# Optimization experiments

Measured on AMD Instinct MI355X. Metric: run time of the kernel, lower is better.

The kernel has to match this reference:

```python
import jax, jax.numpy as jnp
import numpy as np

I = 512  # input_size
H = 512  # hidden_size
L = 512  # sequence length
N = 64   # batch


def setup_inputs() -> dict:
    key = jax.random.key(0)
    ks = jax.random.split(key, 12)
    s_ih = 1.0 / np.sqrt(H)
    inp = {
        "input": jax.random.normal(ks[0], (L, N, I), dtype=jnp.float32),
        "h_0": jax.random.normal(ks[1], (2, N, H), dtype=jnp.float32),
        # layer 0 params
        "W_ih_l0": jax.random.uniform(ks[2], (H, I), jnp.float32, -s_ih, s_ih),
        "W_hh_l0": jax.random.uniform(ks[3], (H, H), jnp.float32, -s_ih, s_ih),
        "b_ih_l0": jax.random.uniform(ks[4], (H,), jnp.float32, -s_ih, s_ih),
        "b_hh_l0": jax.random.uniform(ks[5], (H,), jnp.float32, -s_ih, s_ih),
        # layer 1 params (input is layer 0 hidden state, size H)
        "W_ih_l1": jax.random.uniform(ks[6], (H, H), jnp.float32, -s_ih, s_ih),
        "W_hh_l1": jax.random.uniform(ks[7], (H, H), jnp.float32, -s_ih, s_ih),
        "b_ih_l1": jax.random.uniform(ks[8], (H,), jnp.float32, -s_ih, s_ih),
        "b_hh_l1": jax.random.uniform(ks[9], (H,), jnp.float32, -s_ih, s_ih),
    }
    return inp


def reference(input, h_0, W_ih_l0, W_hh_l0, b_ih_l0, b_hh_l0,
              W_ih_l1, W_hh_l1, b_ih_l1, b_hh_l1):
    """2-layer Elman RNN with tanh: h[t] = tanh(x[t] W_ih^T + b_ih + h[t-1] W_hh^T + b_hh).
    Layer 1 consumes layer 0's hidden state at the same timestep.
    Returns (output: (L, N, H), h_n: (2, N, H)).
    """

    def step(carry, x_t):
        h0, h1 = carry  # each (N, H)
        h0_new = jnp.tanh(x_t @ W_ih_l0.T + b_ih_l0 + h0 @ W_hh_l0.T + b_hh_l0)
        h1_new = jnp.tanh(h0_new @ W_ih_l1.T + b_ih_l1 + h1 @ W_hh_l1.T + b_hh_l1)
        return (h0_new, h1_new), h1_new

    (h0_n, h1_n), output = jax.lax.scan(step, (h_0[0], h_0[1]), input)
    h_n = jnp.stack([h0_n, h1_n], axis=0)
    return output, h_n
```

## Files before the change

kernel.cpp:

```cpp
#include <hip/hip_runtime.h>
#include <hip/hip_bf16.h>
#include <math.h>

#define L_SEQ 512
#define N_B   64
#define H_D   512
#define M_TOT (L_SEQ * N_B)

typedef unsigned short u16;
typedef unsigned long long u64;
typedef __attribute__((ext_vector_type(8))) short short8;
typedef __attribute__((ext_vector_type(4))) float f32x4;
typedef __attribute__((ext_vector_type(4))) int i32x4;
typedef __attribute__((ext_vector_type(2))) int i32x2;

__device__ __forceinline__ u16 f2bf(float f) {
    unsigned int u = __builtin_bit_cast(unsigned int, f);
    u = u + 0x7fffu + ((u >> 16) & 1u);
    return (u16)(u >> 16);
}

__device__ __forceinline__ float fast_tanh(float x) {
    float e = __expf(2.0f * x);
    return 1.0f - 2.0f / (e + 1.0f);
}

__device__ __forceinline__ void st_h(u16* p, u16 v) {
    __hip_atomic_store(p, v, __ATOMIC_RELAXED, __HIP_MEMORY_SCOPE_AGENT);
}
__device__ __forceinline__ void st_flag(int* p, int v) {
    __hip_atomic_store(p, v, __ATOMIC_RELAXED, __HIP_MEMORY_SCOPE_AGENT);
}

#define FSTRIDE 16

#define LD16(f, p)                                                          \
  asm volatile(                                                             \
    "global_load_dwordx4 %0, %16, off\n\t"                                  \
    "global_load_dwordx4 %1, %16, off offset:64\n\t"                        \
    "global_load_dwordx4 %2, %16, off offset:128\n\t"                       \
    "global_load_dwordx4 %3, %16, off offset:192\n\t"                       \
    "global_load_dwordx4 %4, %16, off offset:256\n\t"                       \
    "global_load_dwordx4 %5, %16, off offset:320\n\t"                       \
    "global_load_dwordx4 %6, %16, off offset:384\n\t"                       \
    "global_load_dwordx4 %7, %16, off offset:448\n\t"                       \
    "global_load_dwordx4 %8, %16, off offset:512\n\t"                       \
    "global_load_dwordx4 %9, %16, off offset:576\n\t"                       \
    "global_load_dwordx4 %10, %16, off offset:640\n\t"                      \
    "global_load_dwordx4 %11, %16, off offset:704\n\t"                      \
    "global_load_dwordx4 %12, %16, off offset:768\n\t"                      \
    "global_load_dwordx4 %13, %16, off offset:832\n\t"                      \
    "global_load_dwordx4 %14, %16, off offset:896\n\t"                      \
    "global_load_dwordx4 %15, %16, off offset:960\n\t"                      \
    "s_waitcnt vmcnt(0)"                                                    \
    : "=&v"(f[0]), "=&v"(f[1]), "=&v"(f[2]), "=&v"(f[3]),                   \
      "=&v"(f[4]), "=&v"(f[5]), "=&v"(f[6]), "=&v"(f[7]),                   \
      "=&v"(f[8]), "=&v"(f[9]), "=&v"(f[10]), "=&v"(f[11]),                 \
      "=&v"(f[12]), "=&v"(f[13]), "=&v"(f[14]), "=&v"(f[15])                \
    : "v"(p) : "memory")

#define LD16X2(f, g, p0, p1)                                                \
  asm volatile(                                                             \
    "global_load_dwordx4 %0, %32, off\n\t"                                  \
    "global_load_dwordx4 %16, %33, off\n\t"                                 \
    "global_load_dwordx4 %1, %32, off offset:64\n\t"                        \
    "global_load_dwordx4 %17, %33, off offset:64\n\t"                       \
    "global_load_dwordx4 %2, %32, off offset:128\n\t"                       \
    "global_load_dwordx4 %18, %33, off offset:128\n\t"                      \
    "global_load_dwordx4 %3, %32, off offset:192\n\t"                       \
    "global_load_dwordx4 %19, %33, off offset:192\n\t"                      \
    "global_load_dwordx4 %4, %32, off offset:256\n\t"                       \
    "global_load_dwordx4 %20, %33, off offset:256\n\t"                      \
    "global_load_dwordx4 %5, %32, off offset:320\n\t"                       \
    "global_load_dwordx4 %21, %33, off offset:320\n\t"                      \
    "global_load_dwordx4 %6, %32, off offset:384\n\t"                       \
    "global_load_dwordx4 %22, %33, off offset:384\n\t"                      \
    "global_load_dwordx4 %7, %32, off offset:448\n\t"                       \
    "global_load_dwordx4 %23, %33, off offset:448\n\t"                      \
    "global_load_dwordx4 %8, %32, off offset:512\n\t"                       \
    "global_load_dwordx4 %24, %33, off offset:512\n\t"                      \
    "global_load_dwordx4 %9, %32, off offset:576\n\t"                       \
    "global_load_dwordx4 %25, %33, off offset:576\n\t"                      \
    "global_load_dwordx4 %10, %32, off offset:640\n\t"                      \
    "global_load_dwordx4 %26, %33, off offset:640\n\t"                      \
    "global_load_dwordx4 %11, %32, off offset:704\n\t"                      \
    "global_load_dwordx4 %27, %33, off offset:704\n\t"                      \
    "global_load_dwordx4 %12, %32, off offset:768\n\t"                      \
    "global_load_dwordx4 %28, %33, off offset:768\n\t"                      \
    "global_load_dwordx4 %13, %32, off offset:832\n\t"                      \
    "global_load_dwordx4 %29, %33, off offset:832\n\t"                      \
    "global_load_dwordx4 %14, %32, off offset:896\n\t"                      \
    "global_load_dwordx4 %30, %33, off offset:896\n\t"                      \
    "global_load_dwordx4 %15, %32, off offset:960\n\t"                      \
    "global_load_dwordx4 %31, %33, off offset:960\n\t"                      \
    "s_waitcnt vmcnt(0)"                                                    \
    : "=&v"(f[0]), "=&v"(f[1]), "=&v"(f[2]), "=&v"(f[3]),                   \
      "=&v"(f[4]), "=&v"(f[5]), "=&v"(f[6]), "=&v"(f[7]),                   \
      "=&v"(f[8]), "=&v"(f[9]), "=&v"(f[10]), "=&v"(f[11]),                 \
      "=&v"(f[12]), "=&v"(f[13]), "=&v"(f[14]), "=&v"(f[15]),               \
      "=&v"(g[0]), "=&v"(g[1]), "=&v"(g[2]), "=&v"(g[3]),                   \
      "=&v"(g[4]), "=&v"(g[5]), "=&v"(g[6]), "=&v"(g[7]),                   \
      "=&v"(g[8]), "=&v"(g[9]), "=&v"(g[10]), "=&v"(g[11]),                 \
      "=&v"(g[12]), "=&v"(g[13]), "=&v"(g[14]), "=&v"(g[15])                \
    : "v"(p0), "v"(p1) : "memory")

#define WAITVM asm volatile("s_waitcnt vmcnt(0)" ::: "memory")

__device__ __host__ __forceinline__ int perm32(int j) {
    return (((j >> 3) & 3) << 2) | (j & 3) | (((j >> 2) & 1) << 4);
}

__global__ void k_prep(const float* __restrict__ x,
                       const float* __restrict__ w0ih, const float* __restrict__ w0hh,
                       const float* __restrict__ b0i,  const float* __restrict__ b0h,
                       const float* __restrict__ w1ih, const float* __restrict__ w1hh,
                       const float* __restrict__ b1i,  const float* __restrict__ b1h,
                       u16* __restrict__ xb,
                       u16* __restrict__ w0ihb, u16* __restrict__ w0hhb,
                       u16* __restrict__ w1ihb, u16* __restrict__ w1hhb,
                       float* __restrict__ bias0, float* __restrict__ bias1,
                       int* __restrict__ flags)
{
    const int stride = gridDim.x * blockDim.x;
    const int tid = blockIdx.x * blockDim.x + threadIdx.x;
    for (int i = tid; i < M_TOT * H_D / 4; i += stride) {
        const float4 v = ((const float4*)x)[i];
        ushort4 o;
        o.x = f2bf(v.x); o.y = f2bf(v.y); o.z = f2bf(v.z); o.w = f2bf(v.w);
        ((ushort4*)xb)[i] = o;
    }
    for (int i = tid; i < H_D * H_D; i += stride) {
        const int p  = i & (H_D - 1);
        const int pc = (i & ~(H_D - 1)) | (p & ~31) | perm32(p & 31);
        w0ihb[i] = f2bf(w0ih[i]);
        w0hhb[i] = f2bf(w0hh[pc]);
        w1ihb[i] = f2bf(w1ih[pc]);
        w1hhb[i] = f2bf(w1hh[i]);
    }
    if (tid < H_D) {
        bias0[tid] = b0i[tid] + b0h[tid];
        bias1[tid] = b1i[tid] + b1h[tid];
    }
    if (tid < 48 * FSTRIDE) flags[tid] = 0;
}

__global__ __launch_bounds__(256)
void k_gemm(const u16* __restrict__ A, const u16* __restrict__ W,
            const float* __restrict__ bias, float* __restrict__ out)
{
    __shared__ u16 As[128][40];
    __shared__ u16 Ws[128][40];
    const int m0 = blockIdx.x * 128;
    const int n0 = blockIdx.y * 128;
    const int tid = threadIdx.x;
    const int w = tid >> 6, l = tid & 63, q = l >> 4, lr = l & 15;
    const int mw = (w >> 1) * 64, nw = (w & 1) * 64;
    const int skg = (tid & 3) * 8;
    const int smr = tid >> 2;

    f32x4 acc[4][4];
    #pragma unroll
    for (int i = 0; i < 4; ++i)
        #pragma unroll
        for (int j = 0; j < 4; ++j)
            acc[i][j] = (f32x4){0.f, 0.f, 0.f, 0.f};

    for (int kk = 0; kk < H_D; kk += 32) {
        *(uint4*)&As[smr][skg]      = *(const uint4*)(A + (size_t)(m0 + smr) * H_D + kk + skg);
        *(uint4*)&As[smr + 64][skg] = *(const uint4*)(A + (size_t)(m0 + smr + 64) * H_D + kk + skg);
        *(uint4*)&Ws[smr][skg]      = *(const uint4*)(W + (size_t)(n0 + smr) * H_D + kk + skg);
        *(uint4*)&Ws[smr + 64][skg] = *(const uint4*)(W + (size_t)(n0 + smr + 64) * H_D + kk + skg);
        __syncthreads();
        short8 af[4], bf[4];
        #pragma unroll
        for (int rt = 0; rt < 4; ++rt) af[rt] = *(const short8*)&As[mw + rt*16 + lr][q*8];
        #pragma unroll
        for (int nt = 0; nt < 4; ++nt) bf[nt] = *(const short8*)&Ws[nw + nt*16 + lr][q*8];
        #pragma unroll
        for (int rt = 0; rt < 4; ++rt)
            #pragma unroll
            for (int nt = 0; nt < 4; ++nt)
                acc[rt][nt] = __builtin_amdgcn_mfma_f32_16x16x32_bf16(af[rt], bf[nt], acc[rt][nt], 0, 0, 0);
        __syncthreads();
    }
    #pragma unroll
    for (int nt = 0; nt < 4; ++nt) {
        const int col = n0 + nw + nt*16 + lr;
        const float bv = bias[col];
        #pragma unroll
        for (int rt = 0; rt < 4; ++rt) {
            #pragma unroll
            for (int r = 0; r < 4; ++r) {
                const int row = m0 + mw + rt*16 + q*4 + r;
                out[(size_t)row * H_D + col] = acc[rt][nt][r] + bv;
            }
        }
    }
}

__global__ __launch_bounds__(256, 1)
void k_rec_fused(const u16* __restrict__ Whh0, const u16* __restrict__ Wih1,
                 const u16* __restrict__ Whh1,
                 const float* __restrict__ h_init,
                 const float* __restrict__ pre0,
                 const float* __restrict__ bias1,
                 u16* __restrict__ h0buf, u16* __restrict__ h1buf,
                 float* __restrict__ out, float* __restrict__ hn,
                 int* __restrict__ flags0, int* __restrict__ flags1)
{
    (void)__hip_atomic_load(flags0, __ATOMIC_ACQUIRE, __HIP_MEMORY_SCOPE_AGENT);

    const int tid = threadIdx.x;
    const int w = tid >> 6, l = tid & 63, q = l >> 4, lr = l & 15;
    const int r0 = w * 16;
    const int m = r0 + lr;

    if (blockIdx.x < 16) {
        const int c = blockIdx.x;
        const int nbase = c * 32;
        short8 breg[16][2];
        #pragma unroll
        for (int kt = 0; kt < 16; ++kt)
            #pragma unroll
            for (int nt = 0; nt < 2; ++nt)
                breg[kt][nt] = *(const short8*)(Whh0 + (size_t)(nbase + nt*16 + lr) * H_D + kt*32 + q*8);

        #pragma unroll
        for (int j = 0; j < 8; ++j) {
            int idx = l * 8 + j;
            int row = r0 + (idx >> 5);
            int pos = idx & 31;
            st_h(h0buf + (size_t)row * H_D + nbase + pos,
                 f2bf(h_init[row * H_D + nbase + perm32(pos)]));
        }
        WAITVM;
        __syncthreads();
        if (tid == 0) st_flag(flags0 + c * FSTRIDE, 1);

        for (int t = 0; t < L_SEQ; ++t) {
            const float* pt = pre0 + (size_t)t * (N_B * H_D)
                            + (size_t)(r0 + lr) * H_D + nbase + q*4;
            f32x4 acc0a = *(const f32x4*)pt;
            f32x4 acc1a = *(const f32x4*)(pt + 16);
            f32x4 acc0b = (f32x4){0.f,0.f,0.f,0.f};
            f32x4 acc1b = (f32x4){0.f,0.f,0.f,0.f};
            f32x4 acc0c = (f32x4){0.f,0.f,0.f,0.f};
            f32x4 acc1c = (f32x4){0.f,0.f,0.f,0.f};
            f32x4 acc0d = (f32x4){0.f,0.f,0.f,0.f};
            f32x4 acc1d = (f32x4){0.f,0.f,0.f,0.f};

            if (w == 0) {
                const int* p = flags0 + (l & 15) * FSTRIDE;
                while (true) {
                    int v = __hip_atomic_load(p, __ATOMIC_RELAXED, __HIP_MEMORY_SCOPE_AGENT);
                    if (__all(v >= t + 1)) break;
                }
                asm volatile("" ::: "memory");
            }
            __syncthreads();

            const u16* hs = h0buf + ((size_t)t * N_B + m) * H_D + q*8;
            i32x4 f[16];
            LD16(f, hs);
            #pragma unroll
            for (int kt = 0; kt < 16; kt += 4) {
                acc0a = __builtin_amdgcn_mfma_f32_16x16x32_bf16(breg[kt][0],   __builtin_bit_cast(short8, f[kt]),   acc0a, 0, 0, 0);
                acc1a = __builtin_amdgcn_mfma_f32_16x16x32_bf16(breg[kt][1],   __builtin_bit_cast(short8, f[kt]),   acc1a, 0, 0, 0);
                acc0b = __builtin_amdgcn_mfma_f32_16x16x32_bf16(breg[kt+1][0], __builtin_bit_cast(short8, f[kt+1]), acc0b, 0, 0, 0);
                acc1b = __builtin_amdgcn_mfma_f32_16x16x32_bf16(breg[kt+1][1], __builtin_bit_cast(short8, f[kt+1]), acc1b, 0, 0, 0);
                acc0c = __builtin_amdgcn_mfma_f32_16x16x32_bf16(breg[kt+2][0], __builtin_bit_cast(short8, f[kt+2]), acc0c, 0, 0, 0);
                acc1c = __builtin_amdgcn_mfma_f32_16x16x32_bf16(breg[kt+2][1], __builtin_bit_cast(short8, f[kt+2]), acc1c, 0, 0, 0);
                acc0d = __builtin_amdgcn_mfma_f32_16x16x32_bf16(breg[kt+3][0], __builtin_bit_cast(short8, f[kt+3]), acc0d, 0, 0, 0);
                acc1d = __builtin_amdgcn_mfma_f32_16x16x32_bf16(breg[kt+3][1], __builtin_bit_cast(short8, f[kt+3]), acc1d, 0, 0, 0);
            }
            float v0[4], v1[4];
            #pragma unroll
            for (int r = 0; r < 4; ++r) {
                v0[r] = fast_tanh((acc0a[r] + acc0b[r]) + (acc0c[r] + acc0d[r]));
                v1[r] = fast_tanh((acc1a[r] + acc1b[r]) + (acc1c[r] + acc1d[r]));
            }
            i32x4 dd;
            dd[0] = (int)((unsigned)f2bf(v0[0]) | ((unsigned)f2bf(v0[1]) << 16));
            dd[1] = (int)((unsigned)f2bf(v0[2]) | ((unsigned)f2bf(v0[3]) << 16));
            dd[2] = (int)((unsigned)f2bf(v1[0]) | ((unsigned)f2bf(v1[1]) << 16));
            dd[3] = (int)((unsigned)f2bf(v1[2]) | ((unsigned)f2bf(v1[3]) << 16));
            u16* hd = h0buf + (size_t)(t+1) * (N_B * H_D)
                    + (size_t)(r0 + lr) * H_D + nbase + q*8;
            asm volatile(
                "global_store_dwordx4 %1, %0, off sc1"
                :: "v"(dd), "v"(hd) : "memory");
            WAITVM;
            __syncthreads();
            if (tid == 0) st_flag(flags0 + c * FSTRIDE, t + 2);

            if (t == L_SEQ - 1) {
                f32x4 o0 = {v0[0], v0[1], v0[2], v0[3]};
                f32x4 o1 = {v1[0], v1[1], v1[2], v1[3]};
                *(f32x4*)(hn + (size_t)(r0 + lr) * H_D + nbase + q*4)      = o0;
                *(f32x4*)(hn + (size_t)(r0 + lr) * H_D + nbase + 16 + q*4) = o1;
            }
        }
    } else {
        const int c = blockIdx.x - 16;
        const int nbase = c * 16;
        short8 bregI[16], bregH[16];
        #pragma unroll
        for (int kt = 0; kt < 16; ++kt) {
            bregI[kt] = *(const short8*)(Wih1 + (size_t)(nbase + lr) * H_D + kt*32 + q*8);
            bregH[kt] = *(const short8*)(Whh1 + (size_t)(nbase + lr) * H_D + kt*32 + q*8);
        }
        const f32x4 bv4 = *(const f32x4*)(bias1 + nbase + q*4);

        const float* hi1 = h_init + N_B * H_D;
        #pragma unroll
        for (int j = 0; j < 4; ++j) {
            int idx = l * 4 + j;
            int row = r0 + (idx >> 4);
            int col = nbase + (idx & 15);
            st_h(h1buf + (size_t)row * H_D + col, f2bf(hi1[row * H_D + col]));
        }
        WAITVM;
        __syncthreads();
        if (tid == 0) st_flag(flags1 + c * FSTRIDE, 1);

        for (int t = 0; t < L_SEQ; ++t) {
            if (w == 0) {
                const int* p;
                int need;
                if (l < 16)      { p = flags0 + l * FSTRIDE;        need = t + 2; }
                else if (l < 48) { p = flags1 + (l - 16) * FSTRIDE; need = t + 1; }
                else             { p = flags0;                      need = 0;     }
                while (true) {
                    int v = __hip_atomic_load(p, __ATOMIC_RELAXED, __HIP_MEMORY_SCOPE_AGENT);
                    if (__all(v >= need)) break;
                }
                asm volatile("" ::: "memory");
            }
            __syncthreads();

            const u16* p0 = h0buf + ((size_t)(t+1) * N_B + m) * H_D + q*8;
            const u16* p1 = h1buf + ((size_t)t     * N_B + m) * H_D + q*8;
            i32x4 f[16], g[16];
            LD16X2(f, g, p0, p1);
            f32x4 accA = bv4;
            f32x4 accB = (f32x4){0.f,0.f,0.f,0.f};
            f32x4 accC = (f32x4){0.f,0.f,0.f,0.f};
            f32x4 accD = (f32x4){0.f,0.f,0.f,0.f};
            #pragma unroll
            for (int kt = 0; kt < 16; kt += 2) {
                accA = __builtin_amdgcn_mfma_f32_16x16x32_bf16(bregI[kt],   __builtin_bit_cast(short8, f[kt]),   accA, 0, 0, 0);
                accB = __builtin_amdgcn_mfma_f32_16x16x32_bf16(bregH[kt],   __builtin_bit_cast(short8, g[kt]),   accB, 0, 0, 0);
                accC = __builtin_amdgcn_mfma_f32_16x16x32_bf16(bregI[kt+1], __builtin_bit_cast(short8, f[kt+1]), accC, 0, 0, 0);
                accD = __builtin_amdgcn_mfma_f32_16x16x32_bf16(bregH[kt+1], __builtin_bit_cast(short8, g[kt+1]), accD, 0, 0, 0);
            }
            float v[4];
            #pragma unroll
            for (int r = 0; r < 4; ++r)
                v[r] = fast_tanh((accA[r] + accB[r]) + (accC[r] + accD[r]));
            i32x2 d;
            d[0] = (int)((unsigned)f2bf(v[0]) | ((unsigned)f2bf(v[1]) << 16));
            d[1] = (int)((unsigned)f2bf(v[2]) | ((unsigned)f2bf(v[3]) << 16));
            u16* hd = h1buf + (size_t)(t+1) * (N_B * H_D)
                    + (size_t)(r0 + lr) * H_D + nbase + q*4;
            asm volatile(
                "global_store_dwordx2 %1, %0, off sc1"
                :: "v"(d), "v"(hd) : "memory");
            WAITVM;
            __syncthreads();
            if (tid == 0) st_flag(flags1 + c * FSTRIDE, t + 2);

            f32x4 ov = {v[0], v[1], v[2], v[3]};
            *(f32x4*)(out + (size_t)t * (N_B * H_D)
                      + (size_t)(r0 + lr) * H_D + nbase + q*4) = ov;
            if (t == L_SEQ - 1)
                *(f32x4*)(hn + (size_t)(N_B + r0 + lr) * H_D + nbase + q*4) = ov;
        }
    }
}

extern "C" void kernel_launch(void* const* d_in, const int* in_sizes, int n_in,
                              void* d_out, int out_size, void* d_ws, size_t ws_size,
                              hipStream_t stream)
{
    (void)in_sizes; (void)n_in; (void)out_size; (void)ws_size;
    const float* x    = (const float*)d_in[0];
    const float* h0   = (const float*)d_in[1];
    const float* w0ih = (const float*)d_in[2];
    const float* w0hh = (const float*)d_in[3];
    const float* b0i  = (const float*)d_in[4];
    const float* b0h  = (const float*)d_in[5];
    const float* w1ih = (const float*)d_in[6];
    const float* w1hh = (const float*)d_in[7];
    const float* b1i  = (const float*)d_in[8];
    const float* b1h  = (const float*)d_in[9];
    float* out = (float*)d_out;
    float* hn  = out + (size_t)M_TOT * H_D;

    char* ws = (char*)d_ws;
    size_t off = 0;
    u16* w0ihb = (u16*)(ws + off);   off += (size_t)H_D * H_D * 2;
    u16* w0hhb = (u16*)(ws + off);   off += (size_t)H_D * H_D * 2;
    u16* w1ihb = (u16*)(ws + off);   off += (size_t)H_D * H_D * 2;
    u16* w1hhb = (u16*)(ws + off);   off += (size_t)H_D * H_D * 2;
    float* bias0 = (float*)(ws + off); off += H_D * 4;
    float* bias1 = (float*)(ws + off); off += H_D * 4;
    int* flags   = (int*)(ws + off);   off += 48 * FSTRIDE * 4;
    int* flags0  = flags;
    int* flags1  = flags + 16 * FSTRIDE;
    u16* h0buf   = (u16*)(ws + off);   off += (size_t)(L_SEQ + 1) * N_B * H_D * 2;
    float* pre0  = (float*)(ws + off); off += (size_t)M_TOT * H_D * 4;
    u16* h1buf   = (u16*)(ws + off);   off += (size_t)(L_SEQ + 1) * N_B * H_D * 2;
    u16* xb      = h1buf;

    k_prep<<<2048, 256, 0, stream>>>(x, w0ih, w0hh, b0i, b0h, w1ih, w1hh, b1i, b1h,
                                     xb, w0ihb, w0hhb, w1ihb, w1hhb,
                                     bias0, bias1, flags);
    k_gemm<<<dim3(M_TOT/128, H_D/128), 256, 0, stream>>>(xb, w0ihb, bias0, pre0);
    k_rec_fused<<<48, 256, 0, stream>>>(w0hhb, w1ihb, w1hhb, h0, pre0, bias1,
                                        h0buf, h1buf, out, hn, flags0, flags1);
}
```

Before: 2.935 ms.

## Split recurrence by batch rows so each block owns full hidden state in LDS

Restructures the recurrent kernel so each 512-thread block handles 16 batch rows across all 512 hidden units. It keeps the hidden state in swizzled shared memory and W_hh in registers plus LDS, which removes the per-step cross-block flag waits inside each layer's recurrence. Layer 1's input projection moves to separate blocks that compute h0·W_ih1 into the pre0 buffer and signal through per-warp flags, pipelining the two layers. This trades a wide cross-block dependency every step for a longer serial per-block chain, fewer blocks (24), and heavy register and LDS use.

```diff
diff --git a/kernel.cpp b/kernel.cpp
--- a/kernel.cpp
+++ b/kernel.cpp
@@ -6,6 +6,8 @@
 #define N_B   64
 #define H_D   512
 #define M_TOT (L_SEQ * N_B)
+#define FSTRIDE 16
+#define SMEM_BYTES (16384 + 8 * 16384)
 
 typedef unsigned short u16;
 typedef unsigned long long u64;
@@ -31,8 +33,6 @@
 __device__ __forceinline__ void st_flag(int* p, int v) {
     __hip_atomic_store(p, v, __ATOMIC_RELAXED, __HIP_MEMORY_SCOPE_AGENT);
 }
-
-#define FSTRIDE 16
 
 #define LD16(f, p)                                                          \
   asm volatile(                                                             \
@@ -59,51 +59,6 @@
       "=&v"(f[12]), "=&v"(f[13]), "=&v"(f[14]), "=&v"(f[15])                \
     : "v"(p) : "memory")
 
-#define LD16X2(f, g, p0, p1)                                                \
-  asm volatile(                                                             \
-    "global_load_dwordx4 %0, %32, off\n\t"                                  \
-    "global_load_dwordx4 %16, %33, off\n\t"                                 \
-    "global_load_dwordx4 %1, %32, off offset:64\n\t"                        \
-    "global_load_dwordx4 %17, %33, off offset:64\n\t"                       \
-    "global_load_dwordx4 %2, %32, off offset:128\n\t"                       \
-    "global_load_dwordx4 %18, %33, off offset:128\n\t"                      \
-    "global_load_dwordx4 %3, %32, off offset:192\n\t"                       \
-    "global_load_dwordx4 %19, %33, off offset:192\n\t"                      \
-    "global_load_dwordx4 %4, %32, off offset:256\n\t"                       \
-    "global_load_dwordx4 %20, %33, off offset:256\n\t"                      \
-    "global_load_dwordx4 %5, %32, off offset:320\n\t"                       \
-    "global_load_dwordx4 %21, %33, off offset:320\n\t"                      \
-    "global_load_dwordx4 %6, %32, off offset:384\n\t"                       \
-    "global_load_dwordx4 %22, %33, off offset:384\n\t"                      \
-    "global_load_dwordx4 %7, %32, off offset:448\n\t"                       \
-    "global_load_dwordx4 %23, %33, off offset:448\n\t"                      \
-    "global_load_dwordx4 %8, %32, off offset:512\n\t"                       \
-    "global_load_dwordx4 %24, %33, off offset:512\n\t"                      \
-    "global_load_dwordx4 %9, %32, off offset:576\n\t"                       \
-    "global_load_dwordx4 %25, %33, off offset:576\n\t"                      \
-    "global_load_dwordx4 %10, %32, off offset:640\n\t"                      \
-    "global_load_dwordx4 %26, %33, off offset:640\n\t"                      \
-    "global_load_dwordx4 %11, %32, off offset:704\n\t"                      \
-    "global_load_dwordx4 %27, %33, off offset:704\n\t"                      \
-    "global_load_dwordx4 %12, %32, off offset:768\n\t"                      \
-    "global_load_dwordx4 %28, %33, off offset:768\n\t"                      \
-    "global_load_dwordx4 %13, %32, off offset:832\n\t"                      \
-    "global_load_dwordx4 %29, %33, off offset:832\n\t"                      \
-    "global_load_dwordx4 %14, %32, off offset:896\n\t"                      \
-    "global_load_dwordx4 %30, %33, off offset:896\n\t"                      \
-    "global_load_dwordx4 %15, %32, off offset:960\n\t"                      \
-    "global_load_dwordx4 %31, %33, off offset:960\n\t"                      \
-    "s_waitcnt vmcnt(0)"                                                    \
-    : "=&v"(f[0]), "=&v"(f[1]), "=&v"(f[2]), "=&v"(f[3]),                   \
-      "=&v"(f[4]), "=&v"(f[5]), "=&v"(f[6]), "=&v"(f[7]),                   \
-      "=&v"(f[8]), "=&v"(f[9]), "=&v"(f[10]), "=&v"(f[11]),                 \
-      "=&v"(f[12]), "=&v"(f[13]), "=&v"(f[14]), "=&v"(f[15]),               \
-      "=&v"(g[0]), "=&v"(g[1]), "=&v"(g[2]), "=&v"(g[3]),                   \
-      "=&v"(g[4]), "=&v"(g[5]), "=&v"(g[6]), "=&v"(g[7]),                   \
-      "=&v"(g[8]), "=&v"(g[9]), "=&v"(g[10]), "=&v"(g[11]),                 \
-      "=&v"(g[12]), "=&v"(g[13]), "=&v"(g[14]), "=&v"(g[15])                \
-    : "v"(p0), "v"(p1) : "memory")
-
 #define WAITVM asm volatile("s_waitcnt vmcnt(0)" ::: "memory")
 
 __device__ __host__ __forceinline__ int perm32(int j) {
@@ -133,7 +88,7 @@
         const int p  = i & (H_D - 1);
         const int pc = (i & ~(H_D - 1)) | (p & ~31) | perm32(p & 31);
         w0ihb[i] = f2bf(w0ih[i]);
-        w0hhb[i] = f2bf(w0hh[pc]);
+        w0hhb[i] = f2bf(w0hh[i]);
         w1ihb[i] = f2bf(w1ih[pc]);
         w1hhb[i] = f2bf(w1hh[i]);
     }
@@ -141,7 +96,7 @@
         bias0[tid] = b0i[tid] + b0h[tid];
         bias1[tid] = b1i[tid] + b1h[tid];
     }
-    if (tid < 48 * FSTRIDE) flags[tid] = 0;
+    if (tid < 192 * FSTRIDE) flags[tid] = 0;
 }
 
 __global__ __launch_bounds__(256)
@@ -198,182 +153,244 @@
     }
 }
 
-__global__ __launch_bounds__(256, 1)
-void k_rec_fused(const u16* __restrict__ Whh0, const u16* __restrict__ Wih1,
-                 const u16* __restrict__ Whh1,
-                 const float* __restrict__ h_init,
-                 const float* __restrict__ pre0,
-                 const float* __restrict__ bias1,
-                 u16* __restrict__ h0buf, u16* __restrict__ h1buf,
-                 float* __restrict__ out, float* __restrict__ hn,
-                 int* __restrict__ flags0, int* __restrict__ flags1)
+__global__ __launch_bounds__(512, 2)
+void k_rec(const u16* __restrict__ Whh0, const u16* __restrict__ Wih1p,
+           const u16* __restrict__ Whh1,
+           const float* __restrict__ h_init,
+           float* __restrict__ pre0,
+           const float* __restrict__ bias1,
+           u16* __restrict__ h0buf,
+           float* __restrict__ out, float* __restrict__ hn,
+           int* __restrict__ flags)
 {
-    (void)__hip_atomic_load(flags0, __ATOMIC_ACQUIRE, __HIP_MEMORY_SCOPE_AGENT);
+    extern __shared__ char smem[];
+    int* flag0 = flags;
+    int* flagF = flags + 16 * FSTRIDE;
+    (void)__hip_atomic_load(flags, __ATOMIC_ACQUIRE, __HIP_MEMORY_SCOPE_AGENT);
 
     const int tid = threadIdx.x;
     const int w = tid >> 6, l = tid & 63, q = l >> 4, lr = l & 15;
-    const int r0 = w * 16;
-    const int m = r0 + lr;
-
-    if (blockIdx.x < 16) {
-        const int c = blockIdx.x;
+    const int swz = (lr & 7) << 4;
+    const int blk = blockIdx.x;
+
+    if (blk < 4) {
+        const int b = blk;
+        const int R = b * 16;
+        short8 bregR[16][3];
+        #pragma unroll
+        for (int kt = 0; kt < 16; ++kt)
+            #pragma unroll
+            for (int nt = 0; nt < 3; ++nt)
+                bregR[kt][nt] = *(const short8*)(Whh0 + (size_t)(64*w + nt*16 + lr) * H_D + kt*32 + q*8);
+        char* wl = smem + 16384 + w * 16384;
+        #pragma unroll
+        for (int kt = 0; kt < 16; ++kt) {
+            short8 t3 = *(const short8*)(Whh0 + (size_t)(64*w + 48 + lr) * H_D + kt*32 + q*8);
+            *(short8*)(wl + kt*1024 + (size_t)l*16) = t3;
+        }
+        #pragma unroll
+        for (int j = 0; j < 16; ++j) {
+            int col = 64*w + q*16 + j;
+            *(u16*)(smem + (((size_t)lr*1024 + col*2) ^ swz)) =
+                f2bf(h_init[(R + lr) * H_D + col]);
+        }
+        __syncthreads();
+
+        f32x4 pr[4];
+        #pragma unroll
+        for (int nt = 0; nt < 4; ++nt)
+            pr[nt] = *(const f32x4*)(pre0 + (size_t)(R+lr)*H_D + 64*w + nt*16 + q*4);
+        f32x4 acc[4];
+        #pragma unroll
+        for (int nt = 0; nt < 4; ++nt) acc[nt] = (f32x4){0.f,0.f,0.f,0.f};
+
+        for (int t = 0; t < L_SEQ; ++t) {
+            #pragma unroll
+            for (int kt = 0; kt < 16; ++kt) {
+                short8 hf = *(const short8*)(smem + (((size_t)lr*1024 + kt*64 + q*16) ^ swz));
+                short8 wf = *(const short8*)(wl + kt*1024 + (size_t)l*16);
+                acc[0] = __builtin_amdgcn_mfma_f32_16x16x32_bf16(bregR[kt][0], hf, acc[0], 0,0,0);
+                acc[1] = __builtin_amdgcn_mfma_f32_16x16x32_bf16(bregR[kt][1], hf, acc[1], 0,0,0);
+                acc[2] = __builtin_amdgcn_mfma_f32_16x16x32_bf16(bregR[kt][2], hf, acc[2], 0,0,0);
+                acc[3] = __builtin_amdgcn_mfma_f32_16x16x32_bf16(wf,           hf, acc[3], 0,0,0);
+            }
+            __syncthreads();
+            if (tid == 0 && t > 0) st_flag(flag0 + b*FSTRIDE, t + 1);
+
+            float v[16]; unsigned hb[16];
+            #pragma unroll
+            for (int nt = 0; nt < 4; ++nt)
+                #pragma unroll
+                for (int r = 0; r < 4; ++r) {
+                    v[nt*4+r]  = fast_tanh(acc[nt][r] + pr[nt][r]);
+                    hb[nt*4+r] = f2bf(v[nt*4+r]);
+                }
+            #pragma unroll
+            for (int nt = 0; nt < 4; ++nt) {
+                i32x2 d;
+                d[0] = (int)(hb[nt*4]   | (hb[nt*4+1] << 16));
+                d[1] = (int)(hb[nt*4+2] | (hb[nt*4+3] << 16));
+                *(i32x2*)(smem + (((size_t)lr*1024 + (64*w + nt*16 + q*4)*2) ^ swz)) = d;
+            }
+            __syncthreads();
+
+            i32x4 dA, dB;
+            dA[0] = (int)(hb[0]  | (hb[1]  << 16)); dA[1] = (int)(hb[2]  | (hb[3]  << 16));
+            dA[2] = (int)(hb[4]  | (hb[5]  << 16)); dA[3] = (int)(hb[6]  | (hb[7]  << 16));
+            dB[0] = (int)(hb[8]  | (hb[9]  << 16)); dB[1] = (int)(hb[10] | (hb[11] << 16));
+            dB[2] = (int)(hb[12] | (hb[13] << 16)); dB[3] = (int)(hb[14] | (hb[15] << 16));
+            u16* hd = h0buf + (size_t)(t+1)*(N_B*H_D) + (size_t)(R+lr)*H_D + 64*w + q*8;
+            asm volatile("global_store_dwordx4 %2, %0, off sc1\n\t"
+                         "global_store_dwordx4 %2, %1, off offset:64 sc1"
+                         :: "v"(dA), "v"(dB), "v"(hd) : "memory");
+            if (t == L_SEQ - 1) {
+                #pragma unroll
+                for (int nt = 0; nt < 4; ++nt) {
+                    f32x4 o = {v[nt*4], v[nt*4+1], v[nt*4+2], v[nt*4+3]};
+                    *(f32x4*)(hn + (size_t)(R+lr)*H_D + 64*w + nt*16 + q*4) = o;
+                }
+            }
+            const int tn = (t + 1 < L_SEQ) ? t + 1 : L_SEQ - 1;
+            #pragma unroll
+            for (int nt = 0; nt < 4; ++nt) {
+                pr[nt]  = *(const f32x4*)(pre0 + (size_t)tn*(N_B*H_D) + (size_t)(R+lr)*H_D + 64*w + nt*16 + q*4);
+                acc[nt] = (f32x4){0.f,0.f,0.f,0.f};
+            }
+        }
+        __syncthreads();
+        if (tid == 0) st_flag(flag0 + b*FSTRIDE, L_SEQ + 1);
+    } else if (blk < 20) {
+        if (w >= 4) return;
+        const int c = blk - 4;
         const int nbase = c * 32;
         short8 breg[16][2];
         #pragma unroll
         for (int kt = 0; kt < 16; ++kt)
             #pragma unroll
             for (int nt = 0; nt < 2; ++nt)
-                breg[kt][nt] = *(const short8*)(Whh0 + (size_t)(nbase + nt*16 + lr) * H_D + kt*32 + q*8);
-
-        #pragma unroll
-        for (int j = 0; j < 8; ++j) {
-            int idx = l * 8 + j;
-            int row = r0 + (idx >> 5);
-            int pos = idx & 31;
-            st_h(h0buf + (size_t)row * H_D + nbase + pos,
-                 f2bf(h_init[row * H_D + nbase + perm32(pos)]));
-        }
-        WAITVM;
-        __syncthreads();
-        if (tid == 0) st_flag(flags0 + c * FSTRIDE, 1);
+                breg[kt][nt] = *(const short8*)(Wih1p + (size_t)(nbase + nt*16 + lr) * H_D + kt*32 + q*8);
+        const f32x4 bv0 = *(const f32x4*)(bias1 + nbase + q*4);
+        const f32x4 bv1 = *(const f32x4*)(bias1 + nbase + 16 + q*4);
+        const int m = w*16 + lr;
 
         for (int t = 0; t < L_SEQ; ++t) {
-            const float* pt = pre0 + (size_t)t * (N_B * H_D)
-                            + (size_t)(r0 + lr) * H_D + nbase + q*4;
-            f32x4 acc0a = *(const f32x4*)pt;
-            f32x4 acc1a = *(const f32x4*)(pt + 16);
-            f32x4 acc0b = (f32x4){0.f,0.f,0.f,0.f};
-            f32x4 acc1b = (f32x4){0.f,0.f,0.f,0.f};
-            f32x4 acc0c = (f32x4){0.f,0.f,0.f,0.f};
-            f32x4 acc1c = (f32x4){0.f,0.f,0.f,0.f};
-            f32x4 acc0d = (f32x4){0.f,0.f,0.f,0.f};
-            f32x4 acc1d = (f32x4){0.f,0.f,0.f,0.f};
-
-            if (w == 0) {
-                const int* p = flags0 + (l & 15) * FSTRIDE;
-                while (true) {
-                    int v = __hip_atomic_load(p, __ATOMIC_RELAXED, __HIP_MEMORY_SCOPE_AGENT);
-                    if (__all(v >= t + 1)) break;
-                }
-                asm volatile("" ::: "memory");
-            }
-            __syncthreads();
-
-            const u16* hs = h0buf + ((size_t)t * N_B + m) * H_D + q*8;
+            const int* p = flag0 + w*FSTRIDE;
+            while (true) {
+                int fv = __hip_atomic_load(p, __ATOMIC_RELAXED, __HIP_MEMORY_SCOPE_AGENT);
+                if (__all(fv >= t + 2)) break;
+            }
+            asm volatile("" ::: "memory");
+            const u16* hs = h0buf + ((size_t)(t+1)*N_B + m)*H_D + q*8;
             i32x4 f[16];
             LD16(f, hs);
+            f32x4 a0a = bv0, a1a = bv1;
+            f32x4 a0b = (f32x4){0.f,0.f,0.f,0.f}, a1b = a0b;
+            f32x4 a0c = a0b, a1c = a0b, a0d = a0b, a1d = a0b;
             #pragma unroll
             for (int kt = 0; kt < 16; kt += 4) {
-                acc0a = __builtin_amdgcn_mfma_f32_16x16x32_bf16(breg[kt][0],   __builtin_bit_cast(short8, f[kt]),   acc0a, 0, 0, 0);
-                acc1a = __builtin_amdgcn_mfma_f32_16x16x32_bf16(breg[kt][1],   __builtin_bit_cast(short8, f[kt]),   acc1a, 0, 0, 0);
-                acc0b = __builtin_amdgcn_mfma_f32_16x16x32_bf16(breg[kt+1][0], __builtin_bit_cast(short8, f[kt+1]), acc0b, 0, 0, 0);
-                acc1b = __builtin_amdgcn_mfma_f32_16x16x32_bf16(breg[kt+1][1], __builtin_bit_cast(short8, f[kt+1]), acc1b, 0, 0, 0);
-                acc0c = __builtin_amdgcn_mfma_f32_16x16x32_bf16(breg[kt+2][0], __builtin_bit_cast(short8, f[kt+2]), acc0c, 0, 0, 0);
-                acc1c = __builtin_amdgcn_mfma_f32_16x16x32_bf16(breg[kt+2][1], __builtin_bit_cast(short8, f[kt+2]), acc1c, 0, 0, 0);
-                acc0d = __builtin_amdgcn_mfma_f32_16x16x32_bf16(breg[kt+3][0], __builtin_bit_cast(short8, f[kt+3]), acc0d, 0, 0, 0);
-                acc1d = __builtin_amdgcn_mfma_f32_16x16x32_bf16(breg[kt+3][1], __builtin_bit_cast(short8, f[kt+3]), acc1d, 0, 0, 0);
-            }
-            float v0[4], v1[4];
+                a0a = __builtin_amdgcn_mfma_f32_16x16x32_bf16(breg[kt][0],   __builtin_bit_cast(short8, f[kt]),   a0a, 0,0,0);
+                a1a = __builtin_amdgcn_mfma_f32_16x16x32_bf16(breg[kt][1],   __builtin_bit_cast(short8, f[kt]),   a1a, 0,0,0);
+                a0b = __builtin_amdgcn_mfma_f32_16x16x32_bf16(breg[kt+1][0], __builtin_bit_cast(short8, f[kt+1]), a0b, 0,0,0);
+                a1b = __builtin_amdgcn_mfma_f32_16x16x32_bf16(breg[kt+1][1], __builtin_bit_cast(short8, f[kt+1]), a1b, 0,0,0);
+                a0c = __builtin_amdgcn_mfma_f32_16x16x32_bf16(breg[kt+2][0], __builtin_bit_cast(short8, f[kt+2]), a0c, 0,0,0);
+                a1c = __builtin_amdgcn_mfma_f32_16x16x32_bf16(breg[kt+2][1], __builtin_bit_cast(short8, f[kt+2]), a1c, 0,0,0);
+                a0d = __builtin_amdgcn_mfma_f32_16x16x32_bf16(breg[kt+3][0], __builtin_bit_cast(short8, f[kt+3]), a0d, 0,0,0);
+                a1d = __builtin_amdgcn_mfma_f32_16x16x32_bf16(breg[kt+3][1], __builtin_bit_cast(short8, f[kt+3]), a1d, 0,0,0);
+            }
+            f32x4 s0, s1;
             #pragma unroll
             for (int r = 0; r < 4; ++r) {
-                v0[r] = fast_tanh((acc0a[r] + acc0b[r]) + (acc0c[r] + acc0d[r]));
-                v1[r] = fast_tanh((acc1a[r] + acc1b[r]) + (acc1c[r] + acc1d[r]));
-            }
-            i32x4 dd;
-            dd[0] = (int)((unsigned)f2bf(v0[0]) | ((unsigned)f2bf(v0[1]) << 16));
-            dd[1] = (int)((unsigned)f2bf(v0[2]) | ((unsigned)f2bf(v0[3]) << 16));
-            dd[2] = (int)((unsigned)f2bf(v1[0]) | ((unsigned)f2bf(v1[1]) << 16));
-            dd[3] = (int)((unsigned)f2bf(v1[2]) | ((unsigned)f2bf(v1[3]) << 16));
-            u16* hd = h0buf + (size_t)(t+1) * (N_B * H_D)
-                    + (size_t)(r0 + lr) * H_D + nbase + q*8;
-            asm volatile(
-                "global_store_dwordx4 %1, %0, off sc1"
-                :: "v"(dd), "v"(hd) : "memory");
+                s0[r] = (a0a[r] + a0b[r]) + (a0c[r] + a0d[r]);
+                s1[r] = (a1a[r] + a1b[r]) + (a1c[r] + a1d[r]);
+            }
+            float* fd = pre0 + (size_t)t*(N_B*H_D) + (size_t)m*H_D + nbase + q*4;
+            asm volatile("global_store_dwordx4 %2, %0, off sc1\n\t"
+                         "global_store_dwordx4 %2, %1, off offset:64 sc1"
+                         :: "v"(s0), "v"(s1), "v"(fd) : "memory");
             WAITVM;
+            if (l == 0) st_flag(flagF + (c*4 + w)*FSTRIDE, t + 1);
+        }
+    } else {
+        const int b = blk - 20;
+        const int R = b * 16;
+        short8 bregR[16][3];
+        #pragma unroll
+        for (int kt = 0; kt < 16; ++kt)
+            #pragma unroll
+            for (int nt = 0; nt < 3; ++nt)
+                bregR[kt][nt] = *(const short8*)(Whh1 + (size_t)(64*w + nt*16 + lr) * H_D + kt*32 + q*8);
+        char* wl = smem + 16384 + w * 16384;
+        #pragma unroll
+        for (int kt = 0; kt < 16; ++kt) {
+            short8 t3 = *(const short8*)(Whh1 + (size_t)(64*w + 48 + lr) * H_D + kt*32 + q*8);
+            *(short8*)(wl + kt*1024 + (size_t)l*16) = t3;
+        }
+        const float* hi1 = h_init + N_B * H_D;
+        #pragma unroll
+        for (int j = 0; j < 16; ++j) {
+            int col = 64*w + q*16 + j;
+            *(u16*)(smem + (((size_t)lr*1024 + col*2) ^ swz)) =
+                f2bf(hi1[(R + lr) * H_D + col]);
+        }
+        __syncthreads();
+
+        f32x4 acc[4];
+        #pragma unroll
+        for (int nt = 0; nt < 4; ++nt) acc[nt] = (f32x4){0.f,0.f,0.f,0.f};
+
+        for (int t = 0; t < L_SEQ; ++t) {
+            const int* p = flagF + ((l & 15)*4 + b)*FSTRIDE;
+            while (true) {
+                int fv = __hip_atomic_load(p, __ATOMIC_RELAXED, __HIP_MEMORY_SCOPE_AGENT);
+                if (__all(fv >= t + 1)) break;
+            }
+            asm volatile("" ::: "memory");
+            const float* fp = pre0 + (size_t)t*(N_B*H_D) + (size_t)(R+lr)*H_D + 64*w + q*4;
+            i32x4 fr0, fr1, fr2, fr3;
+            asm volatile("global_load_dwordx4 %0, %4, off sc1\n\t"
+                         "global_load_dwordx4 %1, %4, off offset:64 sc1\n\t"
+                         "global_load_dwordx4 %2, %4, off offset:128 sc1\n\t"
+                         "global_load_dwordx4 %3, %4, off offset:192 sc1"
+                         : "=&v"(fr0), "=&v"(fr1), "=&v"(fr2), "=&v"(fr3)
+                         : "v"(fp) : "memory");
+            #pragma unroll
+            for (int kt = 0; kt < 16; ++kt) {
+                short8 hf = *(const short8*)(smem + (((size_t)lr*1024 + kt*64 + q*16) ^ swz));
+                short8 wf = *(const short8*)(wl + kt*1024 + (size_t)l*16);
+                acc[0] = __builtin_amdgcn_mfma_f32_16x16x32_bf16(bregR[kt][0], hf, acc[0], 0,0,0);
+                acc[1] = __builtin_amdgcn_mfma_f32_16x16x32_bf16(bregR[kt][1], hf, acc[1], 0,0,0);
+                acc[2] = __builtin_amdgcn_mfma_f32_16x16x32_bf16(bregR[kt][2], hf, acc[2], 0,0,0);
+                acc[3] = __builtin_amdgcn_mfma_f32_16x16x32_bf16(wf,           hf, acc[3], 0,0,0);
+            }
+            asm volatile("s_waitcnt vmcnt(0)"
+                         : "+v"(fr0), "+v"(fr1), "+v"(fr2), "+v"(fr3) :: "memory");
+            f32x4 fa[4] = { __builtin_bit_cast(f32x4, fr0), __builtin_bit_cast(f32x4, fr1),
+                            __builtin_bit_cast(f32x4, fr2), __builtin_bit_cast(f32x4, fr3) };
             __syncthreads();
-            if (tid == 0) st_flag(flags0 + c * FSTRIDE, t + 2);
-
-            if (t == L_SEQ - 1) {
-                f32x4 o0 = {v0[0], v0[1], v0[2], v0[3]};
-                f32x4 o1 = {v1[0], v1[1], v1[2], v1[3]};
-                *(f32x4*)(hn + (size_t)(r0 + lr) * H_D + nbase + q*4)      = o0;
-                *(f32x4*)(hn + (size_t)(r0 + lr) * H_D + nbase + 16 + q*4) = o1;
-            }
-        }
-    } else {
-        const int c = blockIdx.x - 16;
-        const int nbase = c * 16;
-        short8 bregI[16], bregH[16];
-        #pragma unroll
-        for (int kt = 0; kt < 16; ++kt) {
-            bregI[kt] = *(const short8*)(Wih1 + (size_t)(nbase + lr) * H_D + kt*32 + q*8);
-            bregH[kt] = *(const short8*)(Whh1 + (size_t)(nbase + lr) * H_D + kt*32 + q*8);
-        }
-        const f32x4 bv4 = *(const f32x4*)(bias1 + nbase + q*4);
-
-        const float* hi1 = h_init + N_B * H_D;
-        #pragma unroll
-        for (int j = 0; j < 4; ++j) {
-            int idx = l * 4 + j;
-            int row = r0 + (idx >> 4);
-            int col = nbase + (idx & 15);
-            st_h(h1buf + (size_t)row * H_D + col, f2bf(hi1[row * H_D + col]));
-        }
-        WAITVM;
-        __syncthreads();
-        if (tid == 0) st_flag(flags1 + c * FSTRIDE, 1);
-
-        for (int t = 0; t < L_SEQ; ++t) {
-            if (w == 0) {
-                const int* p;
-                int need;
-                if (l < 16)      { p = flags0 + l * FSTRIDE;        need = t + 2; }
-                else if (l < 48) { p = flags1 + (l - 16) * FSTRIDE; need = t + 1; }
-                else             { p = flags0;                      need = 0;     }
-                while (true) {
-                    int v = __hip_atomic_load(p, __ATOMIC_RELAXED, __HIP_MEMORY_SCOPE_AGENT);
-                    if (__all(v >= need)) break;
+            float v[16]; unsigned hb[16];
+            #pragma unroll
+            for (int nt = 0; nt < 4; ++nt)
+                #pragma unroll
+                for (int r = 0; r < 4; ++r) {
+                    v[nt*4+r]  = fast_tanh(fa[nt][r] + acc[nt][r]);
+                    hb[nt*4+r] = f2bf(v[nt*4+r]);
                 }
-                asm volatile("" ::: "memory");
+            #pragma unroll
+            for (int nt = 0; nt < 4; ++nt) {
+                i32x2 d;
+                d[0] = (int)(hb[nt*4]   | (hb[nt*4+1] << 16));
+                d[1] = (int)(hb[nt*4+2] | (hb[nt*4+3] << 16));
+                *(i32x2*)(smem + (((size_t)lr*1024 + (64*w + nt*16 + q*4)*2) ^ swz)) = d;
+            }
+            #pragma unroll
+            for (int nt = 0; nt < 4; ++nt) {
+                f32x4 o = {v[nt*4], v[nt*4+1], v[nt*4+2], v[nt*4+3]};
+                *(f32x4*)(out + (size_t)t*(N_B*H_D) + (size_t)(R+lr)*H_D + 64*w + nt*16 + q*4) = o;
+                if (t == L_SEQ - 1)
+                    *(f32x4*)(hn + (size_t)(N_B + R + lr)*H_D + 64*w + nt*16 + q*4) = o;
+                acc[nt] = (f32x4){0.f,0.f,0.f,0.f};
             }
             __syncthreads();
-
-            const u16* p0 = h0buf + ((size_t)(t+1) * N_B + m) * H_D + q*8;
-            const u16* p1 = h1buf + ((size_t)t     * N_B + m) * H_D + q*8;
-            i32x4 f[16], g[16];
-            LD16X2(f, g, p0, p1);
-            f32x4 accA = bv4;
-            f32x4 accB = (f32x4){0.f,0.f,0.f,0.f};
-            f32x4 accC = (f32x4){0.f,0.f,0.f,0.f};
-            f32x4 accD = (f32x4){0.f,0.f,0.f,0.f};
-            #pragma unroll
-            for (int kt = 0; kt < 16; kt += 2) {
-                accA = __builtin_amdgcn_mfma_f32_16x16x32_bf16(bregI[kt],   __builtin_bit_cast(short8, f[kt]),   accA, 0, 0, 0);
-                accB = __builtin_amdgcn_mfma_f32_16x16x32_bf16(bregH[kt],   __builtin_bit_cast(short8, g[kt]),   accB, 0, 0, 0);
-                accC = __builtin_amdgcn_mfma_f32_16x16x32_bf16(bregI[kt+1], __builtin_bit_cast(short8, f[kt+1]), accC, 0, 0, 0);
-                accD = __builtin_amdgcn_mfma_f32_16x16x32_bf16(bregH[kt+1], __builtin_bit_cast(short8, g[kt+1]), accD, 0, 0, 0);
-            }
-            float v[4];
-            #pragma unroll
-            for (int r = 0; r < 4; ++r)
-                v[r] = fast_tanh((accA[r] + accB[r]) + (accC[r] + accD[r]));
-            i32x2 d;
-            d[0] = (int)((unsigned)f2bf(v[0]) | ((unsigned)f2bf(v[1]) << 16));
-            d[1] = (int)((unsigned)f2bf(v[2]) | ((unsigned)f2bf(v[3]) << 16));
-            u16* hd = h1buf + (size_t)(t+1) * (N_B * H_D)
-                    + (size_t)(r0 + lr) * H_D + nbase + q*4;
-            asm volatile(
-                "global_store_dwordx2 %1, %0, off sc1"
-                :: "v"(d), "v"(hd) : "memory");
-            WAITVM;
-            __syncthreads();
-            if (tid == 0) st_flag(flags1 + c * FSTRIDE, t + 2);
-
-            f32x4 ov = {v[0], v[1], v[2], v[3]};
-            *(f32x4*)(out + (size_t)t * (N_B * H_D)
-                      + (size_t)(r0 + lr) * H_D + nbase + q*4) = ov;
-            if (t == L_SEQ - 1)
-                *(f32x4*)(hn + (size_t)(N_B + r0 + lr) * H_D + nbase + q*4) = ov;
         }
     }
 }
@@ -404,18 +421,18 @@
     u16* w1hhb = (u16*)(ws + off);   off += (size_t)H_D * H_D * 2;
     float* bias0 = (float*)(ws + off); off += H_D * 4;
     float* bias1 = (float*)(ws + off); off += H_D * 4;
-    int* flags   = (int*)(ws + off);   off += 48 * FSTRIDE * 4;
-    int* flags0  = flags;
-    int* flags1  = flags + 16 * FSTRIDE;
+    int* flags   = (int*)(ws + off);   off += 192 * FSTRIDE * 4;
     u16* h0buf   = (u16*)(ws + off);   off += (size_t)(L_SEQ + 1) * N_B * H_D * 2;
     float* pre0  = (float*)(ws + off); off += (size_t)M_TOT * H_D * 4;
-    u16* h1buf   = (u16*)(ws + off);   off += (size_t)(L_SEQ + 1) * N_B * H_D * 2;
-    u16* xb      = h1buf;
+    u16* xb      = h0buf;
+
+    (void)hipFuncSetAttribute((const void*)k_rec,
+                              hipFuncAttributeMaxDynamicSharedMemorySize, SMEM_BYTES);
 
     k_prep<<<2048, 256, 0, stream>>>(x, w0ih, w0hh, b0i, b0h, w1ih, w1hh, b1i, b1h,
                                      xb, w0ihb, w0hhb, w1ihb, w1hhb,
                                      bias0, bias1, flags);
     k_gemm<<<dim3(M_TOT/128, H_D/128), 256, 0, stream>>>(xb, w0ihb, bias0, pre0);
-    k_rec_fused<<<48, 256, 0, stream>>>(w0hhb, w1ihb, w1hhb, h0, pre0, bias1,
-                                        h0buf, h1buf, out, hn, flags0, flags1);
-}
+    k_rec<<<24, 512, SMEM_BYTES, stream>>>(w0hhb, w1ihb, w1hhb, h0, pre0, bias1,
+                                           h0buf, out, hn, flags);
+}
```

Measured after the change: 2.645 ms. 1.11x faster.
